# Kernel tuning notes

Measured on AMD Instinct MI355X. Metric: run time of the kernel, lower is better.

## Reference

```python
import jax, jax.numpy as jnp
import numpy as np

D, H, L, P = 256, 8, 3, 4
DH = D // H
SHAPES = np.array([[72, 96], [36, 48], [18, 24]], dtype=np.int64)
STARTS = np.array([0, 72 * 96, 72 * 96 + 36 * 48], dtype=np.int64)
NV = int((SHAPES[:, 0] * SHAPES[:, 1]).sum())  # 9072


def layer_norm(x, s, b):
    m = x.mean(-1, keepdims=True)
    v = ((x - m) ** 2).mean(-1, keepdims=True)
    return (x - m) / jnp.sqrt(v + 1e-5) * s + b


def bilinear(v, loc, Hl, Wl):
    # v: [B,H,Hl*Wl,dh]; loc: [B,Lq,H,P,2] normalized in [0,1]
    B, nH, _, dh = v.shape
    Lq, nP = loc.shape[1], loc.shape[3]
    x = loc[..., 0] * Wl - 0.5  # grid_sample align_corners=False
    y = loc[..., 1] * Hl - 0.5
    x0 = jnp.floor(x); y0 = jnp.floor(y)
    wx = x - x0; wy = y - y0

    def gather(xi, yi, w):
        valid = (xi >= 0) & (xi < Wl) & (yi >= 0) & (yi < Hl)  # padding_mode='zeros'
        xi_c = jnp.clip(xi, 0, Wl - 1).astype(jnp.int32)
        yi_c = jnp.clip(yi, 0, Hl - 1).astype(jnp.int32)
        idx = jnp.transpose(yi_c * Wl + xi_c, (0, 2, 1, 3)).reshape(B, nH, Lq * nP)
        g = jnp.take_along_axis(v, idx[..., None], axis=2).reshape(B, nH, Lq, nP, dh)
        m = (jnp.transpose(valid, (0, 2, 1, 3)).astype(v.dtype) * jnp.transpose(w, (0, 2, 1, 3)))[..., None]
        return g * m

    return (gather(x0, y0, (1 - wx) * (1 - wy)) + gather(x0 + 1, y0, wx * (1 - wy))
            + gather(x0, y0 + 1, (1 - wx) * wy) + gather(x0 + 1, y0 + 1, wx * wy))


def ms_deform_attn(query, value_in, spatial_shapes, level_start_index, key_padding_mask,
                   ref, off_w, off_b, aw_w, aw_b, vproj_w, vproj_b, oproj_w, oproj_b):
    B, Lq, _ = query.shape
    off = (query @ off_w + off_b).reshape(B, Lq, H, L, P, 2)
    aw = jax.nn.softmax((query @ aw_w + aw_b).reshape(B, Lq, H, L * P), axis=-1).reshape(B, Lq, H, L, P)
    # normalizer is [W_l, H_l] per level
    normalizer = jnp.asarray(np.stack([SHAPES[:, 1], SHAPES[:, 0]], axis=-1), dtype=query.dtype)  # [L,2]
    loc = ref[:, :, None, :, None, :] + off / normalizer[None, None, None, :, None, :]  # [B,Lq,H,L,P,2]
    value = value_in @ vproj_w + vproj_b
    value = jnp.where(key_padding_mask[:, :, None], 0.0, value)
    value = value.reshape(B, -1, H, DH).transpose(0, 2, 1, 3)  # [B,H,Nv,dh]
    acc = 0.0
    for l in range(L):
        Hl, Wl = int(spatial_shapes[l][0]), int(spatial_shapes[l][1])
        st = int(level_start_index[l])
        v_l = value[:, :, st:st + Hl * Wl]
        sampled = bilinear(v_l, loc[:, :, :, l], Hl, Wl)  # [B,H,Lq,P,dh]
        acc = acc + (sampled * jnp.transpose(aw[:, :, :, l], (0, 2, 1, 3))[..., None]).sum(axis=3)
    ctx = acc.transpose(0, 2, 1, 3).reshape(B, Lq, D)
    return ctx @ oproj_w + oproj_b


def mha(q_in, kv_in, key_padding_mask, qw, qb, kw, kb, vw, vb, ow, ob):
    B, Lq, _ = q_in.shape
    Lk = kv_in.shape[1]
    q = (q_in @ qw + qb).reshape(B, Lq, H, DH)
    k = (kv_in @ kw + kb).reshape(B, Lk, H, DH)
    v = (kv_in @ vw + vb).reshape(B, Lk, H, DH)
    scores = jnp.einsum('bqhd,bkhd->bhqk', q, k) / jnp.sqrt(jnp.asarray(DH, q.dtype))
    scores = jnp.where(key_padding_mask[:, None, None, :], -1e9, scores)
    a = jax.nn.softmax(scores, axis=-1)
    ctx = jnp.einsum('bhqk,bkhd->bqhd', a, v).reshape(B, Lq, D)
    return ctx @ ow + ob


def _forward(vis_tokens, text_tokens, vis_value,
             ref_w, ref_b, off_w, off_b, aw_w, aw_b, vproj_w, vproj_b, oproj_w, oproj_b,
             lvi_out_w, lvi_out_b, lvi_n1_s, lvi_n1_b, lvi_f1_w, lvi_f1_b, lvi_f2_w, lvi_f2_b, lvi_n2_s, lvi_n2_b,
             mha_qw, mha_qb, mha_kw, mha_kb, mha_vw, mha_vb, mha_ow, mha_ob,
             vli_out_w, vli_out_b, vli_n1_s, vli_n1_b, vli_f1_w, vli_f1_b, vli_f2_w, vli_f2_b, vli_n2_s, vli_n2_b,
             spatial_shapes, level_start_index, text_padding_mask, vis_key_padding_mask):
    B, Lt, _ = text_tokens.shape
    # --- DeformLVI: text queries multi-scale visual features ---
    ref = jax.nn.sigmoid(text_tokens @ ref_w + ref_b).reshape(B, Lt, L, 2)
    ctx = ms_deform_attn(text_tokens, vis_value, spatial_shapes, level_start_index, vis_key_padding_mask,
                         ref, off_w, off_b, aw_w, aw_b, vproj_w, vproj_b, oproj_w, oproj_b)
    t = layer_norm(text_tokens + ctx @ lvi_out_w + lvi_out_b, lvi_n1_s, lvi_n1_b)
    ffn = jax.nn.relu(t @ lvi_f1_w + lvi_f1_b) @ lvi_f2_w + lvi_f2_b
    text_out = layer_norm(t + ffn, lvi_n2_s, lvi_n2_b)
    # --- VLI: visual tokens query enriched text ---
    ctx_v = mha(vis_tokens, text_out, text_padding_mask, mha_qw, mha_qb, mha_kw, mha_kb, mha_vw, mha_vb, mha_ow, mha_ob)
    v = layer_norm(vis_tokens + ctx_v @ vli_out_w + vli_out_b, vli_n1_s, vli_n1_b)
    ffn_v = jax.nn.relu(v @ vli_f1_w + vli_f1_b) @ vli_f2_w + vli_f2_b
    vis_out = layer_norm(v + ffn_v, vli_n2_s, vli_n2_b)
    return vis_out, text_out


def setup_inputs() -> dict:
    key = jax.random.key(0)
    ks = iter(jax.random.split(key, 64))
    B, Lt = 8, 32
    w = lambda i, o: jax.random.normal(next(ks), (i, o), jnp.float32) * 0.02
    z = lambda o: jnp.zeros((o,), jnp.float32)
    inp = {
        'vis_tokens': jax.random.normal(next(ks), (B, NV, D), jnp.float32),
        'text_tokens': jax.random.normal(next(ks), (B, Lt, D), jnp.float32),
        'vis_value': jax.random.normal(next(ks), (B, NV, D), jnp.float32),
        'ref_w': w(D, L * 2), 'ref_b': z(L * 2),
        'off_w': w(D, H * L * P * 2), 'off_b': z(H * L * P * 2),
        'aw_w': w(D, H * L * P), 'aw_b': z(H * L * P),
        'vproj_w': w(D, D), 'vproj_b': z(D),
        'oproj_w': w(D, D), 'oproj_b': z(D),
        'lvi_out_w': w(D, D), 'lvi_out_b': z(D),
        'lvi_n1_s': jnp.ones((D,), jnp.float32), 'lvi_n1_b': z(D),
        'lvi_f1_w': w(D, 4 * D), 'lvi_f1_b': z(4 * D),
        'lvi_f2_w': w(4 * D, D), 'lvi_f2_b': z(D),
        'lvi_n2_s': jnp.ones((D,), jnp.float32), 'lvi_n2_b': z(D),
        'mha_qw': w(D, D), 'mha_qb': z(D),
        'mha_kw': w(D, D), 'mha_kb': z(D),
        'mha_vw': w(D, D), 'mha_vb': z(D),
        'mha_ow': w(D, D), 'mha_ob': z(D),
        'vli_out_w': w(D, D), 'vli_out_b': z(D),
        'vli_n1_s': jnp.ones((D,), jnp.float32), 'vli_n1_b': z(D),
        'vli_f1_w': w(D, 4 * D), 'vli_f1_b': z(4 * D),
        'vli_f2_w': w(4 * D, D), 'vli_f2_b': z(D),
        'vli_n2_s': jnp.ones((D,), jnp.float32), 'vli_n2_b': z(D),
        'spatial_shapes': SHAPES,
        'level_start_index': STARTS,
        'text_padding_mask': jnp.zeros((B, Lt), bool),
        'vis_key_padding_mask': jnp.zeros((B, NV), bool),
    }
    return inp


def reference(vis_tokens, text_tokens, vis_value,
              ref_w, ref_b, off_w, off_b, aw_w, aw_b, vproj_w, vproj_b, oproj_w, oproj_b,
              lvi_out_w, lvi_out_b, lvi_n1_s, lvi_n1_b, lvi_f1_w, lvi_f1_b, lvi_f2_w, lvi_f2_b, lvi_n2_s, lvi_n2_b,
              mha_qw, mha_qb, mha_kw, mha_kb, mha_vw, mha_vb, mha_ow, mha_ob,
              vli_out_w, vli_out_b, vli_n1_s, vli_n1_b, vli_f1_w, vli_f1_b, vli_f2_w, vli_f2_b, vli_n2_s, vli_n2_b,
              spatial_shapes, level_start_index, text_padding_mask, vis_key_padding_mask):
    return _forward(vis_tokens, text_tokens, vis_value,
                    ref_w, ref_b, off_w, off_b, aw_w, aw_b, vproj_w, vproj_b, oproj_w, oproj_b,
                    lvi_out_w, lvi_out_b, lvi_n1_s, lvi_n1_b, lvi_f1_w, lvi_f1_b, lvi_f2_w, lvi_f2_b, lvi_n2_s, lvi_n2_b,
                    mha_qw, mha_qb, mha_kw, mha_kb, mha_vw, mha_vb, mha_ow, mha_ob,
                    vli_out_w, vli_out_b, vli_n1_s, vli_n1_b, vli_f1_w, vli_f1_b, vli_f2_w, vli_f2_b, vli_n2_s, vli_n2_b,
                    spatial_shapes, level_start_index, text_padding_mask, vis_key_padding_mask)
```

## Files before the change

kernel.cpp:

```cpp
#include <hip/hip_runtime.h>
#include <hip/hip_bf16.h>
#include <math.h>

typedef __hip_bfloat16 bf16;
typedef unsigned short ushort_t;
typedef unsigned int uint_t;
typedef short v8s __attribute__((ext_vector_type(8)));
typedef float v4f __attribute__((ext_vector_type(4)));

#define NVTOK 9072
#define BATCH 8
#define LT 32
#define DMODEL 256
#define NHEAD 8
#define DHEAD 32
#define MVIS (BATCH*NVTOK)
#define MTEXT (BATCH*LT)
#define VISSZ 18579456ull

__device__ __forceinline__ float bf2f(ushort_t u){ return __uint_as_float(((uint_t)u)<<16); }
__device__ __forceinline__ ushort_t f2bfbits(float f){
  __hip_bfloat16 h = __float2bfloat16(f);
  union { __hip_bfloat16 h; ushort_t u; } c; c.h = h; return c.u;
}
__device__ __forceinline__ float ldin(const void* p, size_t i, int mode){
  return mode ? ((const float*)p)[i] : bf2f(((const ushort_t*)p)[i]);
}
__device__ __forceinline__ void stout(void* p, size_t i, int mode, float v){
  if (mode) ((float*)p)[i] = v; else ((ushort_t*)p)[i] = f2bfbits(v);
}

__device__ __forceinline__ void gload_lds16(const void* g, void* l){
  __builtin_amdgcn_global_load_lds(
      (const __attribute__((address_space(1))) unsigned int*)g,
      (__attribute__((address_space(3))) unsigned int*)l, 16, 0, 0);
}

__global__ void k_detect(const uint_t* __restrict__ buf, int n_avail, int* __restrict__ flag){
  __shared__ int zc, bc;
  if (threadIdx.x==0){ zc=0; bc=0; }
  __syncthreads();
  int stride = n_avail/2048; if (stride < 1) stride = 1;
  int nz=0, nb=0;
  for (int i=threadIdx.x; i<2048; i+=256){
    long long idx = (long long)i*stride;
    if (idx >= n_avail) break;
    uint_t d = buf[idx];
    uint_t lo = d & 0xFFFFu;
    int e = (int)((lo >> 7) & 0xFF);
    if (lo == 0) nz++;
    else if (e >= 90 && e <= 160) nb++;
  }
  atomicAdd(&zc, nz); atomicAdd(&bc, nb);
  __syncthreads();
  if (threadIdx.x==0){
    int mode;
    if (zc > 1024) mode = 1;
    else if (bc > 1228) mode = 0;
    else mode = 1;
    *flag = mode;
  }
}

__global__ __launch_bounds__(256) void k_transpose(
    const void* W, ushort_t* __restrict__ Wt, int K, int N,
    const int* __restrict__ mf)
{
  const int mode = *mf;
  __shared__ float tile[32][33];
  const int k0 = blockIdx.x*32, n0 = blockIdx.y*32;
  const int c = threadIdx.x & 31, r8 = threadIdx.x >> 5;
  #pragma unroll
  for (int i=0;i<4;i++){
    const int kk = r8 + i*8;
    tile[kk][c] = ldin(W, (size_t)(k0+kk)*N + n0 + c, mode);
  }
  __syncthreads();
  #pragma unroll
  for (int i=0;i<4;i++){
    const int nn = r8 + i*8;
    Wt[(size_t)(n0+nn)*K + k0 + c] = f2bfbits(tile[c][nn]);
  }
}

__global__ __launch_bounds__(256) void k_text_prep(
    const void* text,
    const void* ref_w, const void* ref_b,
    const void* off_w, const void* off_b,
    const void* aw_w,  const void* aw_b,
    float* __restrict__ loc_out, float* __restrict__ aw_out,
    const int* __restrict__ mf)
{
  const int mode = *mf;
  const int r = blockIdx.x;
  const int t = threadIdx.x;
  __shared__ float x[256];
  __shared__ float refv[6];
  __shared__ float offv[192];
  __shared__ float logit[96];
  x[t] = ldin(text, (size_t)r*256 + t, mode);
  __syncthreads();
  if (t < 192) {
    float s = 0.f;
    for (int k=0;k<256;k++) s += x[k]*ldin(off_w, (size_t)k*192+t, mode);
    offv[t] = s + ldin(off_b, t, mode);
  } else if (t < 198) {
    int j = t-192;
    float s = 0.f;
    for (int k=0;k<256;k++) s += x[k]*ldin(ref_w, (size_t)k*6+j, mode);
    s += ldin(ref_b, j, mode);
    refv[j] = 1.f/(1.f+expf(-s));
  }
  if (t < 96) {
    float s = 0.f;
    for (int k=0;k<256;k++) s += x[k]*ldin(aw_w, (size_t)k*96+t, mode);
    logit[t] = s + ldin(aw_b, t, mode);
  }
  __syncthreads();
  if (t < 8) {
    float mx = -1e30f;
    for (int j=0;j<12;j++) mx = fmaxf(mx, logit[t*12+j]);
    float e[12]; float den = 0.f;
    for (int j=0;j<12;j++){ e[j] = expf(logit[t*12+j]-mx); den += e[j]; }
    float inv = 1.f/den;
    for (int j=0;j<12;j++) aw_out[(size_t)r*96 + t*12 + j] = e[j]*inv;
  }
  if (t < 192) {
    int rem = t % 24;
    int l = rem >> 3;
    int c = t & 1;
    const float normW[3] = {96.f,48.f,24.f};
    const float normH[3] = {72.f,36.f,18.f};
    float nrm = (c==0) ? normW[l] : normH[l];
    loc_out[(size_t)r*192 + t] = refv[l*2+c] + offv[t]/nrm;
  }
}

__global__ __launch_bounds__(64) void k_deform(
    const void* vis_value, const char* __restrict__ vmask,
    const void* vproj_w, const void* vproj_b,
    const float* __restrict__ loc, const float* __restrict__ aw,
    float* __restrict__ ctx_out, const int* __restrict__ mf)
{
  const int mode = *mf;
  const int blk = blockIdx.x;
  const int r = blk >> 3;
  const int h = blk & 7;
  const int b = r >> 5;
  const int t = threadIdx.x;
  const int Hs[3] = {72,36,18};
  const int Wsz[3] = {96,48,24};
  const int stl[3] = {0,6912,8640};
  float s0=0.f,s1=0.f,s2=0.f,s3=0.f, wsum=0.f;
  for (int l=0;l<3;l++){
    for (int p=0;p<4;p++){
      const int sIdx = blk*12 + l*4 + p;
      const float a  = aw[sIdx];
      const float X = loc[sIdx*2+0]*(float)Wsz[l] - 0.5f;
      const float Y = loc[sIdx*2+1]*(float)Hs[l] - 0.5f;
      const float x0f = floorf(X), y0f = floorf(Y);
      const int x0 = (int)x0f, y0 = (int)y0f;
      const float wx = X-x0f, wy = Y-y0f;
      const float cw[4] = {(1.f-wx)*(1.f-wy), wx*(1.f-wy), (1.f-wx)*wy, wx*wy};
      const int cx[4] = {x0,x0+1,x0,x0+1};
      const int cy[4] = {y0,y0,y0+1,y0+1};
      for (int c=0;c<4;c++){
        if (cx[c]>=0 && cx[c]<Wsz[l] && cy[c]>=0 && cy[c]<Hs[l]){
          const size_t pos = (size_t)b*NVTOK + stl[l] + cy[c]*Wsz[l] + cx[c];
          if (vmask[pos]) continue;
          const float w = a*cw[c];
          wsum += w;
          const size_t base = pos*256 + t*4;
          s0 += w*ldin(vis_value, base+0, mode);
          s1 += w*ldin(vis_value, base+1, mode);
          s2 += w*ldin(vis_value, base+2, mode);
          s3 += w*ldin(vis_value, base+3, mode);
        }
      }
    }
  }
  __shared__ float sh[256];
  sh[t*4+0]=s0; sh[t*4+1]=s1; sh[t*4+2]=s2; sh[t*4+3]=s3;
  __syncthreads();
  if (t < 32) {
    const int col = h*32 + t;
    float acc = wsum * ldin(vproj_b, col, mode);
    for (int k=0;k<256;k++) acc += sh[k]*ldin(vproj_w, (size_t)k*256+col, mode);
    ctx_out[(size_t)r*256 + col] = acc;
  }
}

__device__ __forceinline__ float block_sum(float v, float* red){
  float sm = v;
  #pragma unroll
  for (int o=32;o>0;o>>=1) sm += __shfl_down(sm,o);
  const int t = threadIdx.x;
  __syncthreads();
  if ((t&63)==0) red[t>>6] = sm;
  __syncthreads();
  return red[0]+red[1]+red[2]+red[3];
}

__global__ __launch_bounds__(256) void k_mgemm(
    const void* A, size_t a_off, int a_kind,
    const ushort_t* __restrict__ Wt, const void* bias, float* __restrict__ C,
    int N, int K, int relu, const int* __restrict__ mf)
{
  const int mode = *mf;
  const int split = (a_kind==1) || (mode==1);
  __shared__ ushort_t Ah[128*32];
  __shared__ ushort_t Al[128*32];
  __shared__ ushort_t Bt[128*32];
  const int tid = threadIdx.x;
  const int gm0 = blockIdx.x*128, gn0 = blockIdx.y*128;
  const int wv = tid>>6, lane = tid&63;
  const int mh = (wv&1)*64, nh = (wv>>1)*64;
  const int r16 = lane&15, q8 = (lane>>4)*8;
  const int srow = tid>>1, sseg = (tid&1)*16;
  v4f acc[4][4];
  #pragma unroll
  for (int i=0;i<4;i++)
    #pragma unroll
    for (int j=0;j<4;j++) acc[i][j] = (v4f){0.f,0.f,0.f,0.f};

  for (int k0=0; k0<K; k0+=32){
    if (k0) __syncthreads();
    {
      const ushort_t* src = Wt + (size_t)(gn0+srow)*K + k0 + sseg;
      ((uint4*)&Bt[srow*32+sseg])[0]   = ((const uint4*)src)[0];
      ((uint4*)&Bt[srow*32+sseg+8])[0] = ((const uint4*)src)[1];
    }
    if (!split){
      const ushort_t* src = (const ushort_t*)A + a_off + (size_t)(gm0+srow)*K + k0 + sseg;
      ((uint4*)&Ah[srow*32+sseg])[0]   = ((const uint4*)src)[0];
      ((uint4*)&Ah[srow*32+sseg+8])[0] = ((const uint4*)src)[1];
    } else {
      const float* src = (const float*)A + a_off + (size_t)(gm0+srow)*K + k0 + sseg;
      #pragma unroll
      for (int v=0;v<4;v++){
        float4 f = ((const float4*)src)[v];
        float xs[4] = {f.x, f.y, f.z, f.w};
        #pragma unroll
        for (int e=0;e<4;e++){
          const int idx = srow*32 + sseg + v*4 + e;
          const ushort_t h = f2bfbits(xs[e]);
          Ah[idx] = h;
          Al[idx] = f2bfbits(xs[e] - bf2f(h));
        }
      }
    }
    __syncthreads();
    v8s af[4], bfr[4], al[4];
    #pragma unroll
    for (int mt=0;mt<4;mt++){
      af[mt] = *(const v8s*)&Ah[(mh + mt*16 + r16)*32 + q8];
      if (split) al[mt] = *(const v8s*)&Al[(mh + mt*16 + r16)*32 + q8];
    }
    #pragma unroll
    for (int nt=0;nt<4;nt++)
      bfr[nt] = *(const v8s*)&Bt[(nh + nt*16 + r16)*32 + q8];
    #pragma unroll
    for (int mt=0;mt<4;mt++){
      #pragma unroll
      for (int nt=0;nt<4;nt++){
        acc[mt][nt] = __builtin_amdgcn_mfma_f32_16x16x32_bf16(af[mt], bfr[nt], acc[mt][nt], 0, 0, 0);
        if (split)
          acc[mt][nt] = __builtin_amdgcn_mfma_f32_16x16x32_bf16(al[mt], bfr[nt], acc[mt][nt], 0, 0, 0);
      }
    }
  }
  const int rq = (lane>>4)*4;
  float bv[4];
  #pragma unroll
  for (int nt=0;nt<4;nt++) bv[nt] = ldin(bias, gn0 + nh + nt*16 + r16, mode);
  #pragma unroll
  for (int mt=0;mt<4;mt++){
    #pragma unroll
    for (int r=0;r<4;r++){
      const size_t ro = (size_t)(gm0 + mh + mt*16 + rq + r)*N + gn0 + nh + r16;
      #pragma unroll
      for (int nt=0;nt<4;nt++){
        float v = acc[mt][nt][r] + bv[nt];
        if (relu) v = fmaxf(v, 0.f);
        C[ro + nt*16] = v;
      }
    }
  }
}

__global__ __launch_bounds__(256) void k_mgemm3(
    const void* A, size_t a_off, int a_kind,
    const ushort_t* __restrict__ Wt, const void* bias,
    float* __restrict__ Cf, ushort_t* __restrict__ Chi,
    int N, int K, int relu, const int* __restrict__ mf)
{
  const int mode = *mf;
  const int rawf32 = (a_kind==0) && (mode==1);
  __shared__ ushort_t Ah[128*32];
  __shared__ ushort_t Bt[128*32];
  const int tid = threadIdx.x;
  const int nbx = gridDim.x, nby = gridDim.y;
  const int total = nbx*nby;
  const int f = blockIdx.y*nbx + blockIdx.x;
  const int qq = total>>3, rr = total&7;
  const int xcd = f&7, pos = f>>3;
  const int wg = (xcd<rr ? xcd*(qq+1) : rr*(qq+1) + (xcd-rr)*qq) + pos;
  const int gm0 = (wg / nby)*128, gn0 = (wg % nby)*128;

  const int wv = tid>>6, lane = tid&63;
  const int mh = (wv&1)*64, nh = (wv>>1)*64;
  const int r16 = lane&15, q8 = (lane>>4)*8;
  const int grow = tid>>2;
  const int gcol = (tid&3)*8;
  const int srow = tid>>1, sseg = (tid&1)*16;
  const ushort_t* Abf = (const ushort_t*)A + a_off;
  v4f acc[4][4];
  #pragma unroll
  for (int i=0;i<4;i++)
    #pragma unroll
    for (int j=0;j<4;j++) acc[i][j] = (v4f){0.f,0.f,0.f,0.f};

  for (int k0=0; k0<K; k0+=32){
    if (k0) __syncthreads();
    gload_lds16(Wt + (size_t)(gn0+grow)*K    + k0 + gcol, &Bt[grow*32      + gcol]);
    gload_lds16(Wt + (size_t)(gn0+grow+64)*K + k0 + gcol, &Bt[(grow+64)*32 + gcol]);
    if (!rawf32){
      gload_lds16(Abf + (size_t)(gm0+grow)*K    + k0 + gcol, &Ah[grow*32      + gcol]);
      gload_lds16(Abf + (size_t)(gm0+grow+64)*K + k0 + gcol, &Ah[(grow+64)*32 + gcol]);
    } else {
      const float* src = (const float*)A + a_off + (size_t)(gm0+srow)*K + k0 + sseg;
      #pragma unroll
      for (int v=0;v<4;v++){
        float4 fq = ((const float4*)src)[v];
        float xs[4] = {fq.x, fq.y, fq.z, fq.w};
        #pragma unroll
        for (int e=0;e<4;e++)
          Ah[srow*32 + sseg + v*4 + e] = f2bfbits(xs[e]);
      }
    }
    __syncthreads();
    v8s af[4], bfr[4];
    #pragma unroll
    for (int mt=0;mt<4;mt++)
      af[mt] = *(const v8s*)&Ah[(mh + mt*16 + r16)*32 + q8];
    #pragma unroll
    for (int nt=0;nt<4;nt++)
      bfr[nt] = *(const v8s*)&Bt[(nh + nt*16 + r16)*32 + q8];
    #pragma unroll
    for (int mt=0;mt<4;mt++){
      #pragma unroll
      for (int nt=0;nt<4;nt++)
        acc[mt][nt] = __builtin_amdgcn_mfma_f32_16x16x32_bf16(af[mt], bfr[nt], acc[mt][nt], 0, 0, 0);
    }
  }
  const int rq = (lane>>4)*4;
  float bv[4];
  #pragma unroll
  for (int nt=0;nt<4;nt++) bv[nt] = ldin(bias, gn0 + nh + nt*16 + r16, mode);
  const int outf = (Cf != nullptr);
  #pragma unroll
  for (int mt=0;mt<4;mt++){
    #pragma unroll
    for (int r=0;r<4;r++){
      const size_t ro = (size_t)(gm0 + mh + mt*16 + rq + r)*N + gn0 + nh + r16;
      #pragma unroll
      for (int nt=0;nt<4;nt++){
        float v = acc[mt][nt][r] + bv[nt];
        if (relu) v = fmaxf(v, 0.f);
        if (outf) Cf[ro + nt*16] = v;
        else      Chi[ro + nt*16] = f2bfbits(v);
      }
    }
  }
}

__global__ __launch_bounds__(256) void k_mgemm_ln(
    const ushort_t* __restrict__ A,
    const ushort_t* __restrict__ Wt, const void* bias,
    const void* RES, size_t res_off, int res_bf16,
    void* OUT, size_t out_off, int out_bf16,
    const void* g, const void* be,
    int K, const int* __restrict__ mf)
{
  const int mode = *mf;
  __shared__ ushort_t Ah[64*32];
  __shared__ ushort_t Bt[256*32];
  __shared__ float rsum[4][64];
  __shared__ float rsq[4][64];
  const int tid = threadIdx.x;
  const int gm0 = blockIdx.x*64;
  const int wv = tid>>6, lane = tid&63;
  const int nh = wv*64;
  const int r16 = lane&15, kq = lane>>4, q8 = kq*8;
  const int grow = tid>>2, gcol = (tid&3)*8;
  v4f acc[4][4];
  #pragma unroll
  for (int i=0;i<4;i++)
    #pragma unroll
    for (int j=0;j<4;j++) acc[i][j] = (v4f){0.f,0.f,0.f,0.f};

  for (int k0=0; k0<K; k0+=32){
    if (k0) __syncthreads();
    gload_lds16(A  + (size_t)(gm0+grow)*K  + k0 + gcol, &Ah[grow*32 + gcol]);
    gload_lds16(Wt + (size_t)grow*K        + k0 + gcol, &Bt[grow*32 + gcol]);
    gload_lds16(Wt + (size_t)(64+grow)*K   + k0 + gcol, &Bt[(64+grow)*32 + gcol]);
    gload_lds16(Wt + (size_t)(128+grow)*K  + k0 + gcol, &Bt[(128+grow)*32 + gcol]);
    gload_lds16(Wt + (size_t)(192+grow)*K  + k0 + gcol, &Bt[(192+grow)*32 + gcol]);
    __syncthreads();
    v8s af[4], bfr[4];
    #pragma unroll
    for (int mt=0;mt<4;mt++)
      af[mt] = *(const v8s*)&Ah[(mt*16 + r16)*32 + q8];
    #pragma unroll
    for (int nt=0;nt<4;nt++)
      bfr[nt] = *(const v8s*)&Bt[(nh + nt*16 + r16)*32 + q8];
    #pragma unroll
    for (int mt=0;mt<4;mt++){
      #pragma unroll
      for (int nt=0;nt<4;nt++)
        acc[mt][nt] = __builtin_amdgcn_mfma_f32_16x16x32_bf16(af[mt], bfr[nt], acc[mt][nt], 0, 0, 0);
    }
  }
  float bv[4];
  #pragma unroll
  for (int nt=0;nt<4;nt++) bv[nt] = ldin(bias, nh + nt*16 + r16, mode);
  #pragma unroll
  for (int mt=0;mt<4;mt++){
    #pragma unroll
    for (int r=0;r<4;r++){
      const int row_l = mt*16 + kq*4 + r;
      const size_t rbase = (size_t)(gm0 + row_l)*256;
      #pragma unroll
      for (int nt=0;nt<4;nt++){
        const int col = nh + nt*16 + r16;
        const float rv = res_bf16 ? bf2f(((const ushort_t*)RES)[res_off + rbase + col])
                                  : ldin(RES, res_off + rbase + col, mode);
        acc[mt][nt][r] = acc[mt][nt][r] + bv[nt] + rv;
      }
    }
  }
  #pragma unroll
  for (int mt=0;mt<4;mt++){
    #pragma unroll
    for (int r=0;r<4;r++){
      float s = acc[mt][0][r] + acc[mt][1][r] + acc[mt][2][r] + acc[mt][3][r];
      #pragma unroll
      for (int o=1;o<16;o<<=1) s += __shfl_xor(s, o);
      if (r16==0) rsum[wv][mt*16 + kq*4 + r] = s;
    }
  }
  __syncthreads();
  float mean[4][4];
  #pragma unroll
  for (int mt=0;mt<4;mt++){
    #pragma unroll
    for (int r=0;r<4;r++){
      const int row_l = mt*16 + kq*4 + r;
      mean[mt][r] = (rsum[0][row_l]+rsum[1][row_l]+rsum[2][row_l]+rsum[3][row_l]) * (1.f/256.f);
    }
  }
  #pragma unroll
  for (int mt=0;mt<4;mt++){
    #pragma unroll
    for (int r=0;r<4;r++){
      const float m = mean[mt][r];
      float s2 = 0.f;
      #pragma unroll
      for (int nt=0;nt<4;nt++){ const float d = acc[mt][nt][r]-m; s2 += d*d; }
      #pragma unroll
      for (int o=1;o<16;o<<=1) s2 += __shfl_xor(s2, o);
      if (r16==0) rsq[wv][mt*16 + kq*4 + r] = s2;
    }
  }
  __syncthreads();
  float gv[4], bev[4];
  #pragma unroll
  for (int nt=0;nt<4;nt++){
    gv[nt]  = ldin(g,  nh + nt*16 + r16, mode);
    bev[nt] = ldin(be, nh + nt*16 + r16, mode);
  }
  #pragma unroll
  for (int mt=0;mt<4;mt++){
    #pragma unroll
    for (int r=0;r<4;r++){
      const int row_l = mt*16 + kq*4 + r;
      const float var = (rsq[0][row_l]+rsq[1][row_l]+rsq[2][row_l]+rsq[3][row_l]) * (1.f/256.f);
      const float inv = rsqrtf(var + 1e-5f);
      const float m = mean[mt][r];
      const size_t obase = (size_t)(gm0 + row_l)*256;
      #pragma unroll
      for (int nt=0;nt<4;nt++){
        const int col = nh + nt*16 + r16;
        const float o = (acc[mt][nt][r]-m)*inv*gv[nt] + bev[nt];
        if (out_bf16) ((ushort_t*)OUT)[obase + col] = f2bfbits(o);
        else          stout(OUT, out_off + obase + col, mode, o);
      }
    }
  }
}

__global__ __launch_bounds__(256) void k_kvsplit(
    const float* __restrict__ kws, const float* __restrict__ vws,
    ushort_t* __restrict__ khi, ushort_t* __restrict__ klo,
    ushort_t* __restrict__ vthi, ushort_t* __restrict__ vtlo)
{
  const int row = blockIdx.x;
  const int b = row >> 5, key = row & 31;
  const int t = threadIdx.x;
  const float f = kws[(size_t)row*256 + t];
  const ushort_t fh = f2bfbits(f);
  khi[(size_t)row*256 + t] = fh;
  klo[(size_t)row*256 + t] = f2bfbits(f - bf2f(fh));
  const float g = vws[(size_t)row*256 + t];
  const ushort_t gh = f2bfbits(g);
  const size_t vt = ((size_t)b*256 + t)*32 + key;
  vthi[vt] = gh;
  vtlo[vt] = f2bfbits(g - bf2f(gh));
}

__global__ __launch_bounds__(256) void k_attn2(
    const ushort_t* __restrict__ qcH,
    ushort_t* __restrict__ aoh,
    const ushort_t* __restrict__ khi, const ushort_t* __restrict__ klo,
    const ushort_t* __restrict__ vthi, const ushort_t* __restrict__ vtlo,
    const char* __restrict__ tmask, int r0)
{
  __shared__ float P[4][16][36];
  const int tid = threadIdx.x;
  const int wv = tid>>6, lane = tid&63;
  const int lrow0 = blockIdx.x*64 + wv*16;
  const int b = (r0 + lrow0)/NVTOK;
  const int m16 = lane&15;
  const int kq = lane>>4;
  const int q8 = kq*8;
  const int key0 = m16, key1 = m16+16;
  const bool msk0 = tmask[b*LT + key0] != 0;
  const bool msk1 = tmask[b*LT + key1] != 0;
  const float scale = 0.17677669529663687f;

  for (int h=0; h<8; ++h){
    const size_t qoff = (size_t)(lrow0 + m16)*256 + h*32 + q8;
    const v8s qh = *(const v8s*)&qcH[qoff];
    const size_t kb0 = ((size_t)(b*32+key0)*256) + h*32 + q8;
    const size_t kb1 = ((size_t)(b*32+key1)*256) + h*32 + q8;
    const v8s kh0 = *(const v8s*)&khi[kb0];
    const v8s kl0 = *(const v8s*)&klo[kb0];
    const v8s kh1 = *(const v8s*)&khi[kb1];
    const v8s kl1 = *(const v8s*)&klo[kb1];
    v4f s0 = (v4f){0.f,0.f,0.f,0.f}, s1 = (v4f){0.f,0.f,0.f,0.f};
    s0 = __builtin_amdgcn_mfma_f32_16x16x32_bf16(qh, kh0, s0, 0,0,0);
    s0 = __builtin_amdgcn_mfma_f32_16x16x32_bf16(qh, kl0, s0, 0,0,0);
    s1 = __builtin_amdgcn_mfma_f32_16x16x32_bf16(qh, kh1, s1, 0,0,0);
    s1 = __builtin_amdgcn_mfma_f32_16x16x32_bf16(qh, kl1, s1, 0,0,0);
    float e0[4], e1[4], inv[4];
    #pragma unroll
    for (int r=0;r<4;r++){
      const float a0 = msk0 ? -1e9f : s0[r]*scale;
      const float a1 = msk1 ? -1e9f : s1[r]*scale;
      float mx = fmaxf(a0,a1);
      #pragma unroll
      for (int o=1;o<16;o<<=1) mx = fmaxf(mx, __shfl_xor(mx,o));
      const float x0 = __expf(a0-mx), x1 = __expf(a1-mx);
      float dn = x0+x1;
      #pragma unroll
      for (int o=1;o<16;o<<=1) dn += __shfl_xor(dn,o);
      e0[r]=x0; e1[r]=x1; inv[r] = 1.f/dn;
    }
    #pragma unroll
    for (int r=0;r<4;r++){
      P[wv][kq*4+r][key0] = e0[r];
      P[wv][kq*4+r][key1] = e1[r];
    }
    __syncthreads();
    float pv[8];
    *(float4*)&pv[0] = *(const float4*)&P[wv][m16][q8];
    *(float4*)&pv[4] = *(const float4*)&P[wv][m16][q8+4];
    v8s ph;
    #pragma unroll
    for (int j=0;j<8;j++) ph[j] = (short)f2bfbits(pv[j]);
    const size_t vb0 = ((size_t)(b*256 + h*32 + m16)*32) + q8;
    const size_t vb1 = ((size_t)(b*256 + h*32 + 16 + m16)*32) + q8;
    const v8s vh0 = *(const v8s*)&vthi[vb0];
    const v8s vl0 = *(const v8s*)&vtlo[vb0];
    const v8s vh1 = *(const v8s*)&vthi[vb1];
    const v8s vl1 = *(const v8s*)&vtlo[vb1];
    v4f o0 = (v4f){0.f,0.f,0.f,0.f}, o1 = (v4f){0.f,0.f,0.f,0.f};
    o0 = __builtin_amdgcn_mfma_f32_16x16x32_bf16(ph, vh0, o0, 0,0,0);
    o0 = __builtin_amdgcn_mfma_f32_16x16x32_bf16(ph, vl0, o0, 0,0,0);
    o1 = __builtin_amdgcn_mfma_f32_16x16x32_bf16(ph, vh1, o1, 0,0,0);
    o1 = __builtin_amdgcn_mfma_f32_16x16x32_bf16(ph, vl1, o1, 0,0,0);
    __syncthreads();
    #pragma unroll
    for (int r=0;r<4;r++){
      const size_t ro = (size_t)(lrow0 + kq*4 + r)*256 + h*32;
      aoh[ro + m16]      = f2bfbits(o0[r]*inv[r]);
      aoh[ro + 16 + m16] = f2bfbits(o1[r]*inv[r]);
    }
  }
}

__global__ __launch_bounds__(256) void k_add_ln(
    const float* __restrict__ X, const void* R, size_t r_off, int r_f32,
    void* OUT, size_t o_off, int o_f32,
    void* OUT2, size_t o2_off,
    const void* g, const void* be, const int* __restrict__ mf)
{
  const int mode = *mf;
  const int row = blockIdx.x; const int t = threadIdx.x;
  const size_t idx = (size_t)row*256 + t;
  __shared__ float red[4];
  const float rv = r_f32 ? ((const float*)R)[r_off+idx] : ldin(R, r_off+idx, mode);
  const float v = X[idx] + rv;
  const float m = block_sum(v, red) * (1.f/256.f);
  __syncthreads();
  const float d = v - m;
  const float var = block_sum(d*d, red) * (1.f/256.f);
  const float o = d*rsqrtf(var+1e-5f)*ldin(g,t,mode) + ldin(be,t,mode);
  if (o_f32) ((float*)OUT)[o_off+idx] = o;
  else       stout(OUT, o_off+idx, mode, o);
  if (OUT2)  stout(OUT2, o2_off+idx, mode, o);
}

__global__ __launch_bounds__(256) void k_add_ln_pres(
    const float* __restrict__ X,
    const ushort_t* __restrict__ RH,
    void* OUT, size_t o_off,
    const void* g, const void* be, const int* __restrict__ mf)
{
  const int mode = *mf;
  const int row = blockIdx.x; const int t = threadIdx.x;
  const size_t idx = (size_t)row*256 + t;
  __shared__ float red[4];
  const float rv = bf2f(RH[idx]);
  const float v = X[idx] + rv;
  const float m = block_sum(v, red) * (1.f/256.f);
  __syncthreads();
  const float d = v - m;
  const float var = block_sum(d*d, red) * (1.f/256.f);
  const float o = d*rsqrtf(var+1e-5f)*ldin(g,t,mode) + ldin(be,t,mode);
  stout(OUT, o_off+idx, mode, o);
}

extern "C" void kernel_launch(void* const* d_in, const int* in_sizes, int n_in,
                              void* d_out, int out_size, void* d_ws, size_t ws_size,
                              hipStream_t stream)
{
  (void)n_in; (void)out_size;
  const void* vis_tokens = d_in[0];
  const void* text_tokens= d_in[1];
  const void* vis_value  = d_in[2];
  const void* ref_w = d_in[3];  const void* ref_b = d_in[4];
  const void* off_w = d_in[5];  const void* off_b = d_in[6];
  const void* aw_w  = d_in[7];  const void* aw_b  = d_in[8];
  const void* vproj_w = d_in[9];  const void* vproj_b = d_in[10];
  const void* oproj_w = d_in[11]; const void* oproj_b = d_in[12];
  const void* lvi_out_w = d_in[13]; const void* lvi_out_b = d_in[14];
  const void* lvi_n1_s = d_in[15];  const void* lvi_n1_b = d_in[16];
  const void* lvi_f1_w = d_in[17];  const void* lvi_f1_b = d_in[18];
  const void* lvi_f2_w = d_in[19];  const void* lvi_f2_b = d_in[20];
  const void* lvi_n2_s = d_in[21];  const void* lvi_n2_b = d_in[22];
  const void* mha_qw = d_in[23]; const void* mha_qb = d_in[24];
  const void* mha_kw = d_in[25]; const void* mha_kb = d_in[26];
  const void* mha_vw = d_in[27]; const void* mha_vb = d_in[28];
  const void* mha_ow = d_in[29]; const void* mha_ob = d_in[30];
  const void* vli_out_w = d_in[31]; const void* vli_out_b = d_in[32];
  const void* vli_n1_s = d_in[33];  const void* vli_n1_b = d_in[34];
  const void* vli_f1_w = d_in[35];  const void* vli_f1_b = d_in[36];
  const void* vli_f2_w = d_in[37];  const void* vli_f2_b = d_in[38];
  const void* vli_n2_s = d_in[39];  const void* vli_n2_b = d_in[40];
  const char* tmask = (const char*)d_in[43];
  const char* vmask = (const char*)d_in[44];

  char* ws = (char*)d_ws;
  int*   flag    = (int*)  (ws + 0);
  float* loc_ws  = (float*)(ws + 256);
  float* aw_ws   = (float*)(ws + 196864);
  float* ctxt_ws = (float*)(ws + 295168);
  float* t_ws    = (float*)(ws + 557312);
  float* tout_ws = (float*)(ws + 819456);
  float* k_ws    = (float*)(ws + 1081600);
  float* v_ws    = (float*)(ws + 1343744);
  ushort_t* wtq  = (ushort_t*)(ws + 1605888ull);
  ushort_t* wto  = (ushort_t*)(ws + 1736960ull);
  ushort_t* wtf1 = (ushort_t*)(ws + 1868032ull);
  ushort_t* wtf2 = (ushort_t*)(ws + 2392320ull);
  ushort_t* wtk   = (ushort_t*)(ws + 2916608ull);
  ushort_t* wtv   = (ushort_t*)(ws + 3047680ull);
  ushort_t* wtop  = (ushort_t*)(ws + 3178752ull);
  ushort_t* wtlo  = (ushort_t*)(ws + 3309824ull);
  ushort_t* wtlf1 = (ushort_t*)(ws + 3440896ull);
  ushort_t* wtlf2 = (ushort_t*)(ws + 3965184ull);
  float* hbuf_t   = (float*)(ws + 4489472ull);
  float* ybuf     = (float*)(ws + 5538048ull);
  float* fbuf     = (float*)(ws + 5800192ull);
  ushort_t* khi   = (ushort_t*)(ws + 6062336ull);
  ushort_t* klo   = (ushort_t*)(ws + 6193408ull);
  ushort_t* vthi  = (ushort_t*)(ws + 6324480ull);
  ushort_t* vtlo  = (ushort_t*)(ws + 6455552ull);
  const size_t fe = 6586624ull;

  long long R_ll = 128;
  if (ws_size > fe) R_ll = (long long)((ws_size - fe) / 3584ull);
  if (R_ll > (long long)MVIS) R_ll = MVIS;
  R_ll &= ~127LL;
  if (R_ll < 128) R_ll = 128;
  const int R = (int)R_ll;
  ushort_t* qcH  = (ushort_t*)(ws + fe);
  float*    ubuf = (float*)   (ws + fe);
  ushort_t* v1H  = (ushort_t*)(ws + fe + (size_t)R*1024ull);
  ushort_t* hbH  = (ushort_t*)(ws + fe + (size_t)R*1536ull);
  ushort_t* aoH  = hbH;

  int ndw = in_sizes[1]/2; if (ndw < 1) ndw = 1;
  k_detect<<<1,256,0,stream>>>((const uint_t*)text_tokens, ndw, flag);

  k_transpose<<<dim3(8,8),  256,0,stream>>>(mha_qw,    wtq,   256, 256,  flag);
  k_transpose<<<dim3(8,8),  256,0,stream>>>(mha_ow,    wto,   256, 256,  flag);
  k_transpose<<<dim3(8,32), 256,0,stream>>>(vli_f1_w,  wtf1,  256, 1024, flag);
  k_transpose<<<dim3(32,8), 256,0,stream>>>(vli_f2_w,  wtf2,  1024, 256, flag);
  k_transpose<<<dim3(8,8),  256,0,stream>>>(mha_kw,    wtk,   256, 256,  flag);
  k_transpose<<<dim3(8,8),  256,0,stream>>>(mha_vw,    wtv,   256, 256,  flag);
  k_transpose<<<dim3(8,8),  256,0,stream>>>(oproj_w,   wtop,  256, 256,  flag);
  k_transpose<<<dim3(8,8),  256,0,stream>>>(lvi_out_w, wtlo,  256, 256,  flag);
  k_transpose<<<dim3(8,32), 256,0,stream>>>(lvi_f1_w,  wtlf1, 256, 1024, flag);
  k_transpose<<<dim3(32,8), 256,0,stream>>>(lvi_f2_w,  wtlf2, 1024, 256, flag);

  k_text_prep<<<MTEXT,256,0,stream>>>(text_tokens, ref_w, ref_b, off_w, off_b,
                                      aw_w, aw_b, loc_ws, aw_ws, flag);
  k_deform<<<MTEXT*NHEAD,64,0,stream>>>(vis_value, vmask, vproj_w, vproj_b,
                                        loc_ws, aw_ws, ctxt_ws, flag);

  {
    dim3 g22(2,2);
    k_mgemm<<<g22,256,0,stream>>>(ctxt_ws, 0, 1, wtop, oproj_b, ybuf, 256, 256, 0, flag);
    k_mgemm<<<g22,256,0,stream>>>(ybuf,    0, 1, wtlo, lvi_out_b, fbuf, 256, 256, 0, flag);
    k_add_ln<<<MTEXT,256,0,stream>>>(fbuf, text_tokens, 0, 0,
                                     t_ws, 0, 1, nullptr, 0, lvi_n1_s, lvi_n1_b, flag);
  }
  {
    dim3 g28(2,8), g22(2,2);
    k_mgemm<<<g28,256,0,stream>>>(t_ws,   0, 1, wtlf1, lvi_f1_b, hbuf_t, 1024, 256, 1, flag);
    k_mgemm<<<g22,256,0,stream>>>(hbuf_t, 0, 1, wtlf2, lvi_f2_b, fbuf,   256, 1024, 0, flag);
    k_add_ln<<<MTEXT,256,0,stream>>>(fbuf, t_ws, 0, 1,
                                     tout_ws, 0, 1, d_out, VISSZ, lvi_n2_s, lvi_n2_b, flag);
  }
  {
    dim3 g22(2,2);
    k_mgemm<<<g22,256,0,stream>>>(tout_ws, 0, 1, wtk, mha_kb, k_ws, 256, 256, 0, flag);
    k_mgemm<<<g22,256,0,stream>>>(tout_ws, 0, 1, wtv, mha_vb, v_ws, 256, 256, 0, flag);
    k_kvsplit<<<256,256,0,stream>>>(k_ws, v_ws, khi, klo, vthi, vtlo);
  }

  for (int r0 = 0; r0 < MVIS; r0 += R){
    const int nr = (MVIS - r0 < R) ? (MVIS - r0) : R;
    dim3 g2(nr/128, 2), g8(nr/128, 8);
    k_mgemm3<<<g2,256,0,stream>>>(vis_tokens, (size_t)r0*256, 0,
                                  wtq, mha_qb, nullptr, qcH, 256, 256, 0, flag);
    k_attn2<<<nr/64,256,0,stream>>>(qcH, aoH, khi, klo, vthi, vtlo, tmask, r0);
    k_mgemm_ln<<<nr/64,256,0,stream>>>(aoH, wto, mha_ob,
                                       vis_tokens, (size_t)r0*256, 0,
                                       v1H, 0, 1,
                                       vli_n1_s, vli_n1_b, 256, flag);
    k_mgemm3<<<g8,256,0,stream>>>(v1H, 0, 2,
                                  wtf1, vli_f1_b, nullptr, hbH, 1024, 256, 1, flag);
    k_mgemm3<<<g2,256,0,stream>>>(hbH, 0, 2,
                                  wtf2, vli_f2_b, ubuf, nullptr, 256, 1024, 0, flag);
    k_add_ln_pres<<<nr,256,0,stream>>>(ubuf, v1H,
                                       d_out, (size_t)r0*256, vli_n2_s, vli_n2_b, flag);
  }
}
```

Measured before the change: 881.2 us.

## Double GEMM K-tile to 64 and XOR-swizzle LDS layout to avoid bank conflicts

The main bf16 MFMA GEMM now stages 64-wide K slices per iteration instead of 32. This halves the number of barrier-separated load/compute rounds. LDS rows are stored with an XOR swizzle on the 8-element segment index, which is meant to remove bank conflicts when lanes read 16-byte fragments along rows of stride 64. It doubles shared memory per block, which may lower occupancy, and it assumes K is a multiple of 64.

```diff
diff --git a/kernel.cpp b/kernel.cpp
--- a/kernel.cpp
+++ b/kernel.cpp
@@ -296,8 +296,8 @@
 {
   const int mode = *mf;
   const int rawf32 = (a_kind==0) && (mode==1);
-  __shared__ ushort_t Ah[128*32];
-  __shared__ ushort_t Bt[128*32];
+  __shared__ ushort_t Ah[128*64];
+  __shared__ ushort_t Bt[128*64];
   const int tid = threadIdx.x;
   const int nbx = gridDim.x, nby = gridDim.y;
   const int total = nbx*nby;
@@ -309,10 +309,10 @@
 
   const int wv = tid>>6, lane = tid&63;
   const int mh = (wv&1)*64, nh = (wv>>1)*64;
-  const int r16 = lane&15, q8 = (lane>>4)*8;
-  const int grow = tid>>2;
-  const int gcol = (tid&3)*8;
-  const int srow = tid>>1, sseg = (tid&1)*16;
+  const int r16 = lane&15, kq = lane>>4;
+  const int sr = tid>>3;
+  const int sg = tid&7;
+  const int srow = tid>>1, chalf = (tid&1)*32;
   const ushort_t* Abf = (const ushort_t*)A + a_off;
   v4f acc[4][4];
   #pragma unroll
@@ -320,40 +320,59 @@
     #pragma unroll
     for (int j=0;j<4;j++) acc[i][j] = (v4f){0.f,0.f,0.f,0.f};
 
-  for (int k0=0; k0<K; k0+=32){
+  for (int k0=0; k0<K; k0+=64){
     if (k0) __syncthreads();
-    gload_lds16(Wt + (size_t)(gn0+grow)*K    + k0 + gcol, &Bt[grow*32      + gcol]);
-    gload_lds16(Wt + (size_t)(gn0+grow+64)*K + k0 + gcol, &Bt[(grow+64)*32 + gcol]);
+    #pragma unroll
+    for (int i=0;i<4;i++){
+      const int r = i*32 + sr;
+      const int gs = (sg ^ (r&7))*8;
+      gload_lds16(Wt + (size_t)(gn0+r)*K + k0 + gs, &Bt[r*64 + sg*8]);
+    }
     if (!rawf32){
-      gload_lds16(Abf + (size_t)(gm0+grow)*K    + k0 + gcol, &Ah[grow*32      + gcol]);
-      gload_lds16(Abf + (size_t)(gm0+grow+64)*K + k0 + gcol, &Ah[(grow+64)*32 + gcol]);
+      #pragma unroll
+      for (int i=0;i<4;i++){
+        const int r = i*32 + sr;
+        const int gs = (sg ^ (r&7))*8;
+        gload_lds16(Abf + (size_t)(gm0+r)*K + k0 + gs, &Ah[r*64 + sg*8]);
+      }
     } else {
-      const float* src = (const float*)A + a_off + (size_t)(gm0+srow)*K + k0 + sseg;
-      #pragma unroll
-      for (int v=0;v<4;v++){
+      const float* src = (const float*)A + a_off + (size_t)(gm0+srow)*K + k0 + chalf;
+      #pragma unroll
+      for (int v=0;v<8;v++){
         float4 fq = ((const float4*)src)[v];
         float xs[4] = {fq.x, fq.y, fq.z, fq.w};
         #pragma unroll
-        for (int e=0;e<4;e++)
-          Ah[srow*32 + sseg + v*4 + e] = f2bfbits(xs[e]);
+        for (int e=0;e<4;e++){
+          const int c = chalf + v*4 + e;
+          const int idx = srow*64 + (((c>>3) ^ (srow&7))<<3) + (c&7);
+          Ah[idx] = f2bfbits(xs[e]);
+        }
       }
     }
     __syncthreads();
-    v8s af[4], bfr[4];
-    #pragma unroll
-    for (int mt=0;mt<4;mt++)
-      af[mt] = *(const v8s*)&Ah[(mh + mt*16 + r16)*32 + q8];
-    #pragma unroll
-    for (int nt=0;nt<4;nt++)
-      bfr[nt] = *(const v8s*)&Bt[(nh + nt*16 + r16)*32 + q8];
-    #pragma unroll
-    for (int mt=0;mt<4;mt++){
-      #pragma unroll
-      for (int nt=0;nt<4;nt++)
-        acc[mt][nt] = __builtin_amdgcn_mfma_f32_16x16x32_bf16(af[mt], bfr[nt], acc[mt][nt], 0, 0, 0);
-    }
-  }
-  const int rq = (lane>>4)*4;
+    #pragma unroll
+    for (int kk=0;kk<2;kk++){
+      const int seg = kk*4 + kq;
+      v8s af[4], bfr[4];
+      #pragma unroll
+      for (int mt=0;mt<4;mt++){
+        const int row = mh + mt*16 + r16;
+        af[mt] = *(const v8s*)&Ah[row*64 + ((seg ^ (row&7))<<3)];
+      }
+      #pragma unroll
+      for (int nt=0;nt<4;nt++){
+        const int row = nh + nt*16 + r16;
+        bfr[nt] = *(const v8s*)&Bt[row*64 + ((seg ^ (row&7))<<3)];
+      }
+      #pragma unroll
+      for (int mt=0;mt<4;mt++){
+        #pragma unroll
+        for (int nt=0;nt<4;nt++)
+          acc[mt][nt] = __builtin_amdgcn_mfma_f32_16x16x32_bf16(af[mt], bfr[nt], acc[mt][nt], 0, 0, 0);
+      }
+    }
+  }
+  const int rq = kq*4;
   float bv[4];
   #pragma unroll
   for (int nt=0;nt<4;nt++) bv[nt] = ldin(bias, gn0 + nh + nt*16 + r16, mode);
```

Result: no change. 868.4 us (-1.5%).
